# Optimization experiments

Measured on AMD Instinct MI355X. Metric: run time of the kernel, lower is better.

Reference implementation:

```python
import jax, jax.numpy as jnp
import numpy as np

TEMPERATURE = 0.1

def setup_inputs() -> dict:
    key = jax.random.key(0)
    k1, k2 = jax.random.split(key)
    z_i = jax.random.normal(k1, (4096, 128), dtype=jnp.float32)
    z_j = jax.random.normal(k2, (4096, 128), dtype=jnp.float32)
    return {"z_i": z_i, "z_j": z_j}

def reference(z_i, z_j):
    n = z_i.shape[0]
    reps = jnp.concatenate([z_i, z_j], axis=0)              # (2N, D)
    # cosine similarity via normalize + GEMM (same math as broadcasted CosineSimilarity,
    # torch eps=1e-8 on the norm)
    norms = jnp.maximum(jnp.linalg.norm(reps, axis=1, keepdims=True), 1e-8)
    rn = reps / norms
    sim = rn @ rn.T                                          # (2N, 2N)
    l_pos = jnp.diagonal(sim, offset=n)                      # (N,)
    r_pos = jnp.diagonal(sim, offset=-n)                     # (N,)
    positives = jnp.concatenate([l_pos, r_pos])[:, None]     # (2N, 1)
    # NOTE: original code's mask bug makes `negatives` the FULL sim matrix
    logits = jnp.concatenate([positives, sim], axis=1) / TEMPERATURE  # (2N, 2N+1)
    # cross-entropy with label 0, reduction='sum'
    log_probs = jax.nn.log_softmax(logits, axis=1)
    loss = -jnp.sum(log_probs[:, 0])
    return loss / (2 * n)
```

## Files before the change

kernel.cpp:

```cpp
#include <hip/hip_runtime.h>
#include <hip/hip_bf16.h>

typedef __bf16 bf16x8 __attribute__((ext_vector_type(8)));
typedef __bf16 bf16x2 __attribute__((ext_vector_type(2)));
typedef float f32x4 __attribute__((ext_vector_type(4)));

#define NROWS 8192
#define HALF_N 4096
#define DIM 128
#define ROW_BYTES 256
#define TINV 10.0f
#define C1 14.42695040888963f
#define LN2 0.6931471805599453f
#define COL_SPLITS 16

#define SWZ(r, kc) ((kc) ^ ((r) & 7))

__global__ __launch_bounds__(256) void k_normalize(
    const float* __restrict__ zi, const float* __restrict__ zj,
    char* __restrict__ rn, float* __restrict__ rowsum)
{
    const int row  = blockIdx.x * 4 + (threadIdx.x >> 6);
    const int lane = threadIdx.x & 63;
    const float* src = (row < HALF_N) ? (zi + (size_t)row * DIM)
                                      : (zj + (size_t)(row - HALF_N) * DIM);
    float2 v = *(const float2*)(src + lane * 2);
    float ss = v.x * v.x + v.y * v.y;
    #pragma unroll
    for (int m = 32; m >= 1; m >>= 1) ss += __shfl_xor(ss, m, 64);
    const float scale = 1.0f / fmaxf(sqrtf(ss), 1e-8f);
    bf16x2 o; o[0] = (__bf16)(v.x * scale); o[1] = (__bf16)(v.y * scale);
    char* dst = rn + (size_t)row * ROW_BYTES + SWZ(row, lane >> 2) * 16 + (lane & 3) * 4;
    *(bf16x2*)dst = o;
    if (blockIdx.x < 32) rowsum[blockIdx.x * 256 + threadIdx.x] = 0.0f;
}

__global__ __launch_bounds__(256) void k_simsum(
    const char* __restrict__ rn, float* __restrict__ rowsum)
{
    __shared__ char lds[128 * ROW_BYTES];
    const int tid  = threadIdx.x;
    const int wave = tid >> 6;
    const int lane = tid & 63;
    const int tile_m = blockIdx.x * 128;
    const int w0 = wave & 1, w1 = wave >> 1;
    const int qrow = lane >> 4;
    const int lcol = lane & 15;

    {
        const char* gA = rn + (size_t)tile_m * ROW_BYTES;
        #pragma unroll
        for (int i = 0; i < 8; ++i) {
            const int off = wave * 8192 + i * 1024;
            __builtin_amdgcn_global_load_lds(
                (const __attribute__((address_space(1))) void*)(gA + off + lane * 16),
                (__attribute__((address_space(3))) void*)(lds + off),
                16, 0, 0);
        }
    }
    __syncthreads();

    bf16x8 afrag[4][4];
    #pragma unroll
    for (int mi = 0; mi < 4; ++mi) {
        const int m = w1 * 64 + mi * 16 + lcol;
        #pragma unroll
        for (int ks = 0; ks < 4; ++ks)
            afrag[mi][ks] = *(const bf16x8*)(lds + m * ROW_BYTES + SWZ(m, ks * 4 + qrow) * 16);
    }
    __syncthreads();

    float rsum[4][4];
    #pragma unroll
    for (int mi = 0; mi < 4; ++mi)
        #pragma unroll
        for (int r = 0; r < 4; ++r) rsum[mi][r] = 0.0f;

    const int col_base = blockIdx.y * (NROWS / COL_SPLITS);
    const int iters = (NROWS / COL_SPLITS) / 128;
    for (int it = 0; it < iters; ++it) {
        const char* gB = rn + (size_t)(col_base + it * 128) * ROW_BYTES;
        #pragma unroll
        for (int i = 0; i < 8; ++i) {
            const int off = wave * 8192 + i * 1024;
            __builtin_amdgcn_global_load_lds(
                (const __attribute__((address_space(1))) void*)(gB + off + lane * 16),
                (__attribute__((address_space(3))) void*)(lds + off),
                16, 0, 0);
        }
        __syncthreads();

        f32x4 acc[4][4];
        const f32x4 zero = {0.0f, 0.0f, 0.0f, 0.0f};
        #pragma unroll
        for (int mi = 0; mi < 4; ++mi)
            #pragma unroll
            for (int ni = 0; ni < 4; ++ni) acc[mi][ni] = zero;

        #pragma unroll
        for (int ks = 0; ks < 4; ++ks) {
            bf16x8 bfrag[4];
            #pragma unroll
            for (int ni = 0; ni < 4; ++ni) {
                const int n = w0 * 64 + ni * 16 + lcol;
                bfrag[ni] = *(const bf16x8*)(lds + n * ROW_BYTES + SWZ(n, ks * 4 + qrow) * 16);
            }
            #pragma unroll
            for (int mi = 0; mi < 4; ++mi)
                #pragma unroll
                for (int ni = 0; ni < 4; ++ni)
                    acc[mi][ni] = __builtin_amdgcn_mfma_f32_16x16x32_bf16(
                        afrag[mi][ks], bfrag[ni], acc[mi][ni], 0, 0, 0);
        }
        __syncthreads();

        #pragma unroll
        for (int mi = 0; mi < 4; ++mi)
            #pragma unroll
            for (int ni = 0; ni < 4; ++ni)
                #pragma unroll
                for (int r = 0; r < 4; ++r)
                    rsum[mi][r] += __builtin_amdgcn_exp2f(acc[mi][ni][r] * C1 - C1);
    }

    #pragma unroll
    for (int mi = 0; mi < 4; ++mi)
        #pragma unroll
        for (int r = 0; r < 4; ++r) {
            float v = rsum[mi][r];
            v += __shfl_xor(v, 1, 64);
            v += __shfl_xor(v, 2, 64);
            v += __shfl_xor(v, 4, 64);
            v += __shfl_xor(v, 8, 64);
            if (lcol == 0)
                atomicAdd(&rowsum[tile_m + w1 * 64 + mi * 16 + qrow * 4 + r], v);
        }
}

__global__ __launch_bounds__(256) void k_finalize(
    const char* __restrict__ rn, const float* __restrict__ rowsum,
    float* __restrict__ row_loss)
{
    const int row  = blockIdx.x * 4 + (threadIdx.x >> 6);
    const int lane = threadIdx.x & 63;
    const int partner = (row + HALF_N) & (NROWS - 1);
    const __bf16* a = (const __bf16*)(rn + (size_t)row * ROW_BYTES
                         + SWZ(row, lane >> 2) * 16 + (lane & 3) * 4);
    const __bf16* b = (const __bf16*)(rn + (size_t)partner * ROW_BYTES
                         + SWZ(partner, lane >> 2) * 16 + (lane & 3) * 4);
    float p = (float)a[0] * (float)b[0] + (float)a[1] * (float)b[1];
    #pragma unroll
    for (int m = 32; m >= 1; m >>= 1) p += __shfl_xor(p, m, 64);
    if (lane == 0) {
        float s = rowsum[row] + __builtin_amdgcn_exp2f(p * C1 - C1);
        row_loss[row] = TINV + __builtin_amdgcn_logf(s) * LN2 - TINV * p;
    }
}

__global__ __launch_bounds__(256) void k_reduce(
    const float* __restrict__ row_loss, float* __restrict__ out)
{
    const f32x4* v4 = (const f32x4*)row_loss;
    float s = 0.0f;
    for (int i = threadIdx.x; i < NROWS / 4; i += 256) {
        f32x4 v = v4[i];
        s += (v[0] + v[1]) + (v[2] + v[3]);
    }
    #pragma unroll
    for (int m = 32; m >= 1; m >>= 1) s += __shfl_xor(s, m, 64);
    __shared__ float part[4];
    if ((threadIdx.x & 63) == 0) part[threadIdx.x >> 6] = s;
    __syncthreads();
    if (threadIdx.x == 0)
        out[0] = (part[0] + part[1] + part[2] + part[3]) * (1.0f / (float)NROWS);
}

extern "C" void kernel_launch(void* const* d_in, const int* in_sizes, int n_in,
                              void* d_out, int out_size, void* d_ws, size_t ws_size,
                              hipStream_t stream)
{
    const float* zi = (const float*)d_in[0];
    const float* zj = (const float*)d_in[1];
    float* out = (float*)d_out;

    char*  rn       = (char*)d_ws;
    float* rowsum   = (float*)((char*)d_ws + (size_t)NROWS * ROW_BYTES);
    float* row_loss = rowsum + NROWS;

    k_normalize<<<NROWS / 4, 256, 0, stream>>>(zi, zj, rn, rowsum);
    k_simsum<<<dim3(NROWS / 128, COL_SPLITS), 256, 0, stream>>>(rn, rowsum);
    k_finalize<<<NROWS / 4, 256, 0, stream>>>(rn, rowsum, row_loss);
    k_reduce<<<1, 256, 0, stream>>>(row_loss, out);
}
```

Baseline: 105.0 us.

## Drop LDS staging in sim GEMM, read B fragments directly from global

Removes LDS staging and barriers from the similarity GEMM. Each wave now owns 64 rows and streams 16-row B fragments straight from global/L2 into registers over 512 columns, with no swizzle. The A operand is pre-scaled by log2(e)/T in a second normalized copy, so the exp step drops its multiply-subtract (no max subtraction, which is safe because the cosine is at most 1). The row-loss formula is rewritten to match. This trades LDS reuse across waves for more redundant global reads, and adds an extra 2 MB workspace copy.

```diff
diff --git a/kernel.cpp b/kernel.cpp
--- a/kernel.cpp
+++ b/kernel.cpp
@@ -9,66 +9,52 @@
 #define HALF_N 4096
 #define DIM 128
 #define ROW_BYTES 256
-#define TINV 10.0f
 #define C1 14.42695040888963f
 #define LN2 0.6931471805599453f
-#define COL_SPLITS 16
-
-#define SWZ(r, kc) ((kc) ^ ((r) & 7))
 
 __global__ __launch_bounds__(256) void k_normalize(
     const float* __restrict__ zi, const float* __restrict__ zj,
-    char* __restrict__ rn, float* __restrict__ rowsum)
+    char* __restrict__ rn, char* __restrict__ rnA, float* __restrict__ rowsum)
 {
-    const int row  = blockIdx.x * 4 + (threadIdx.x >> 6);
+    const int wave = threadIdx.x >> 6;
     const int lane = threadIdx.x & 63;
-    const float* src = (row < HALF_N) ? (zi + (size_t)row * DIM)
-                                      : (zj + (size_t)(row - HALF_N) * DIM);
-    float2 v = *(const float2*)(src + lane * 2);
-    float ss = v.x * v.x + v.y * v.y;
     #pragma unroll
-    for (int m = 32; m >= 1; m >>= 1) ss += __shfl_xor(ss, m, 64);
-    const float scale = 1.0f / fmaxf(sqrtf(ss), 1e-8f);
-    bf16x2 o; o[0] = (__bf16)(v.x * scale); o[1] = (__bf16)(v.y * scale);
-    char* dst = rn + (size_t)row * ROW_BYTES + SWZ(row, lane >> 2) * 16 + (lane & 3) * 4;
-    *(bf16x2*)dst = o;
-    if (blockIdx.x < 32) rowsum[blockIdx.x * 256 + threadIdx.x] = 0.0f;
+    for (int i = 0; i < 4; ++i) {
+        const int row = blockIdx.x * 16 + wave * 4 + i;
+        const float* src = (row < HALF_N) ? (zi + (size_t)row * DIM)
+                                          : (zj + (size_t)(row - HALF_N) * DIM);
+        float2 v = *(const float2*)(src + lane * 2);
+        float ss = v.x * v.x + v.y * v.y;
+        #pragma unroll
+        for (int m = 32; m >= 1; m >>= 1) ss += __shfl_xor(ss, m, 64);
+        const float sc = 1.0f / fmaxf(sqrtf(ss), 1e-8f);
+        bf16x2 a, b;
+        a[0] = (__bf16)(v.x * sc);      a[1] = (__bf16)(v.y * sc);
+        b[0] = (__bf16)(v.x * sc * C1); b[1] = (__bf16)(v.y * sc * C1);
+        *(bf16x2*)(rn  + (size_t)row * ROW_BYTES + lane * 4) = a;
+        *(bf16x2*)(rnA + (size_t)row * ROW_BYTES + lane * 4) = b;
+    }
+    if (threadIdx.x < 16) rowsum[blockIdx.x * 16 + threadIdx.x] = 0.0f;
 }
 
-__global__ __launch_bounds__(256) void k_simsum(
-    const char* __restrict__ rn, float* __restrict__ rowsum)
+__global__ __launch_bounds__(256) void k_gemm(
+    const char* __restrict__ rn, const char* __restrict__ rnA,
+    float* __restrict__ rowsum)
 {
-    __shared__ char lds[128 * ROW_BYTES];
-    const int tid  = threadIdx.x;
-    const int wave = tid >> 6;
-    const int lane = tid & 63;
-    const int tile_m = blockIdx.x * 128;
-    const int w0 = wave & 1, w1 = wave >> 1;
-    const int qrow = lane >> 4;
-    const int lcol = lane & 15;
+    const int wave = threadIdx.x >> 6;
+    const int lane = threadIdx.x & 63;
+    const int qrow = lane >> 4, lcol = lane & 15;
+    const int cv = blockIdx.x & 15;
+    const int rg = (blockIdx.x >> 4) * 4 + wave;
 
-    {
-        const char* gA = rn + (size_t)tile_m * ROW_BYTES;
-        #pragma unroll
-        for (int i = 0; i < 8; ++i) {
-            const int off = wave * 8192 + i * 1024;
-            __builtin_amdgcn_global_load_lds(
-                (const __attribute__((address_space(1))) void*)(gA + off + lane * 16),
-                (__attribute__((address_space(3))) void*)(lds + off),
-                16, 0, 0);
-        }
-    }
-    __syncthreads();
-
+    const char* Ab = rnA + (size_t)(rg * 64) * ROW_BYTES;
     bf16x8 afrag[4][4];
     #pragma unroll
-    for (int mi = 0; mi < 4; ++mi) {
-        const int m = w1 * 64 + mi * 16 + lcol;
+    for (int mi = 0; mi < 4; ++mi)
         #pragma unroll
         for (int ks = 0; ks < 4; ++ks)
-            afrag[mi][ks] = *(const bf16x8*)(lds + m * ROW_BYTES + SWZ(m, ks * 4 + qrow) * 16);
-    }
-    __syncthreads();
+            afrag[mi][ks] = *(const bf16x8*)(Ab + (mi * 16 + lcol) * ROW_BYTES
+                                             + ks * 64 + qrow * 16);
 
     float rsum[4][4];
     #pragma unroll
@@ -76,51 +62,32 @@
         #pragma unroll
         for (int r = 0; r < 4; ++r) rsum[mi][r] = 0.0f;
 
-    const int col_base = blockIdx.y * (NROWS / COL_SPLITS);
-    const int iters = (NROWS / COL_SPLITS) / 128;
-    for (int it = 0; it < iters; ++it) {
-        const char* gB = rn + (size_t)(col_base + it * 128) * ROW_BYTES;
+    const char* Bb = rn + (size_t)(cv * 512) * ROW_BYTES + lcol * ROW_BYTES + qrow * 16;
+
+    #pragma unroll 1
+    for (int s = 0; s < 32; ++s) {
+        const char* bp = Bb + s * 16 * ROW_BYTES;
+        bf16x8 bfrag[4];
         #pragma unroll
-        for (int i = 0; i < 8; ++i) {
-            const int off = wave * 8192 + i * 1024;
-            __builtin_amdgcn_global_load_lds(
-                (const __attribute__((address_space(1))) void*)(gB + off + lane * 16),
-                (__attribute__((address_space(3))) void*)(lds + off),
-                16, 0, 0);
-        }
-        __syncthreads();
+        for (int ks = 0; ks < 4; ++ks)
+            bfrag[ks] = *(const bf16x8*)(bp + ks * 64);
 
-        f32x4 acc[4][4];
+        f32x4 acc[4];
         const f32x4 zero = {0.0f, 0.0f, 0.0f, 0.0f};
         #pragma unroll
-        for (int mi = 0; mi < 4; ++mi)
-            #pragma unroll
-            for (int ni = 0; ni < 4; ++ni) acc[mi][ni] = zero;
-
+        for (int mi = 0; mi < 4; ++mi) acc[mi] = zero;
         #pragma unroll
-        for (int ks = 0; ks < 4; ++ks) {
-            bf16x8 bfrag[4];
-            #pragma unroll
-            for (int ni = 0; ni < 4; ++ni) {
-                const int n = w0 * 64 + ni * 16 + lcol;
-                bfrag[ni] = *(const bf16x8*)(lds + n * ROW_BYTES + SWZ(n, ks * 4 + qrow) * 16);
-            }
+        for (int ks = 0; ks < 4; ++ks)
             #pragma unroll
             for (int mi = 0; mi < 4; ++mi)
-                #pragma unroll
-                for (int ni = 0; ni < 4; ++ni)
-                    acc[mi][ni] = __builtin_amdgcn_mfma_f32_16x16x32_bf16(
-                        afrag[mi][ks], bfrag[ni], acc[mi][ni], 0, 0, 0);
-        }
-        __syncthreads();
+                acc[mi] = __builtin_amdgcn_mfma_f32_16x16x32_bf16(
+                    afrag[mi][ks], bfrag[ks], acc[mi], 0, 0, 0);
 
         #pragma unroll
         for (int mi = 0; mi < 4; ++mi)
             #pragma unroll
-            for (int ni = 0; ni < 4; ++ni)
-                #pragma unroll
-                for (int r = 0; r < 4; ++r)
-                    rsum[mi][r] += __builtin_amdgcn_exp2f(acc[mi][ni][r] * C1 - C1);
+            for (int r = 0; r < 4; ++r)
+                rsum[mi][r] += __builtin_amdgcn_exp2f(acc[mi][r]);
     }
 
     #pragma unroll
@@ -133,27 +100,26 @@
             v += __shfl_xor(v, 4, 64);
             v += __shfl_xor(v, 8, 64);
             if (lcol == 0)
-                atomicAdd(&rowsum[tile_m + w1 * 64 + mi * 16 + qrow * 4 + r], v);
+                atomicAdd(&rowsum[rg * 64 + mi * 16 + qrow * 4 + r], v);
         }
 }
 
-__global__ __launch_bounds__(256) void k_finalize(
+__global__ __launch_bounds__(256) void k_rowloss(
     const char* __restrict__ rn, const float* __restrict__ rowsum,
     float* __restrict__ row_loss)
 {
     const int row  = blockIdx.x * 4 + (threadIdx.x >> 6);
     const int lane = threadIdx.x & 63;
     const int partner = (row + HALF_N) & (NROWS - 1);
-    const __bf16* a = (const __bf16*)(rn + (size_t)row * ROW_BYTES
-                         + SWZ(row, lane >> 2) * 16 + (lane & 3) * 4);
-    const __bf16* b = (const __bf16*)(rn + (size_t)partner * ROW_BYTES
-                         + SWZ(partner, lane >> 2) * 16 + (lane & 3) * 4);
+    const bf16x2 a = *(const bf16x2*)(rn + (size_t)row * ROW_BYTES + lane * 4);
+    const bf16x2 b = *(const bf16x2*)(rn + (size_t)partner * ROW_BYTES + lane * 4);
     float p = (float)a[0] * (float)b[0] + (float)a[1] * (float)b[1];
     #pragma unroll
     for (int m = 32; m >= 1; m >>= 1) p += __shfl_xor(p, m, 64);
     if (lane == 0) {
-        float s = rowsum[row] + __builtin_amdgcn_exp2f(p * C1 - C1);
-        row_loss[row] = TINV + __builtin_amdgcn_logf(s) * LN2 - TINV * p;
+        const float pc = p * C1;
+        const float S  = rowsum[row] + __builtin_amdgcn_exp2f(pc);
+        row_loss[row] = (__builtin_amdgcn_logf(S) - pc) * LN2;
     }
 }
 
@@ -184,11 +150,12 @@
     float* out = (float*)d_out;
 
     char*  rn       = (char*)d_ws;
-    float* rowsum   = (float*)((char*)d_ws + (size_t)NROWS * ROW_BYTES);
+    char*  rnA      = rn + (size_t)NROWS * ROW_BYTES;
+    float* rowsum   = (float*)(rnA + (size_t)NROWS * ROW_BYTES);
     float* row_loss = rowsum + NROWS;
 
-    k_normalize<<<NROWS / 4, 256, 0, stream>>>(zi, zj, rn, rowsum);
-    k_simsum<<<dim3(NROWS / 128, COL_SPLITS), 256, 0, stream>>>(rn, rowsum);
-    k_finalize<<<NROWS / 4, 256, 0, stream>>>(rn, rowsum, row_loss);
+    k_normalize<<<NROWS / 16, 256, 0, stream>>>(zi, zj, rn, rnA, rowsum);
+    k_gemm<<<512, 256, 0, stream>>>(rn, rnA, rowsum);
+    k_rowloss<<<NROWS / 4, 256, 0, stream>>>(rn, rowsum, row_loss);
     k_reduce<<<1, 256, 0, stream>>>(row_loss, out);
 }
```

Measured after the change: 102.9 us. -2.0%, faster.
